# Kernel optimization log

Measured on AMD Instinct MI355X. Metric: run time of the kernel, lower is better.

## Reference

```python
import jax, jax.numpy as jnp
import numpy as np

IMAGE_SIZE = 256  # init kwarg image_size
BS, NCAM, N = 2, 3, 128


def _normalise_scale_factor(v):
    v = v / v.mean()
    sf = 0.2 / jnp.abs(v - 1.0).max()
    return jnp.where(sf < 1.0, (v - 1.0) * sf + 1.0, v)


def setup_inputs() -> dict:
    key = jax.random.key(0)
    ks = jax.random.split(key, 7)
    S = IMAGE_SIZE
    # 2D projected points in pixel coords [0, S)
    points = jax.random.uniform(ks[0], (BS, NCAM, N, 2), dtype=jnp.float32) * S
    # per-point render params in the model's clamp ranges
    sigmas = jax.random.uniform(ks[1], (BS, N), dtype=jnp.float32) * 0.06 + 0.041
    exponents = jax.random.uniform(ks[2], (BS, N), dtype=jnp.float32) * 1.5 + 0.5
    intensities = jax.random.uniform(ks[3], (BS, N), dtype=jnp.float32) * 0.6 + 0.41
    # per-camera scale factors near 1
    camera_sigmas = jax.random.uniform(ks[4], (BS, NCAM), dtype=jnp.float32) * 0.2 + 0.9
    camera_exponents = jax.random.uniform(ks[5], (BS, NCAM), dtype=jnp.float32) * 0.2 + 0.9
    camera_intensities = jax.random.uniform(ks[6], (BS, NCAM), dtype=jnp.float32) * 0.2 + 0.9
    return {
        'points': points, 'sigmas': sigmas, 'exponents': exponents,
        'intensities': intensities, 'camera_sigmas': camera_sigmas,
        'camera_exponents': camera_exponents, 'camera_intensities': camera_intensities,
    }


def reference(points, sigmas, exponents, intensities,
              camera_sigmas, camera_exponents, camera_intensities):
    S = IMAGE_SIZE
    bs, N = points.shape[0], points.shape[2]
    s2 = S // 2
    # normalise pixel coords to [-1, 1], flatten cameras into batch
    p = jnp.clip((points - s2) / s2, -1.0, 1.0).reshape(bs * 3, N, 2)
    # camera scale factors (normalised as in forward())
    cs = _normalise_scale_factor(camera_sigmas).reshape(bs * 3)
    ce = _normalise_scale_factor(camera_exponents).reshape(bs * 3)
    ci = _normalise_scale_factor(camera_intensities).reshape(bs * 3)
    # repeat_interleave(3, 0) over batch -> (bs*3, N, 1, 1)
    sig = (jnp.repeat(sigmas, 3, axis=0) * cs[:, None])[:, :, None, None]
    expn = (jnp.repeat(exponents, 3, axis=0) * ce[:, None])[:, :, None, None]
    inten = (jnp.repeat(intensities, 3, axis=0) * ci[:, None])[:, :, None, None]
    grid = jnp.linspace(-1.0, 1.0, S, dtype=jnp.float32)
    px = p[:, :, 0][:, :, None, None]  # (bs3, N, 1, 1)
    py = p[:, :, 1][:, :, None, None]
    # squared distance of every point to every pixel: (bs3, N, S, S)
    # y varies over axis -2 (rows), x over axis -1 (cols), matching meshgrid(ij)
    dst = (grid[None, None, None, :] - px) ** 2 + (grid[None, None, :, None] - py) ** 2
    blobs = jnp.exp(-(dst / (2.0 * sig ** 2)) ** expn)
    masks = jnp.minimum((blobs * inten).max(axis=1), 1.0)  # amax over N points
    masks = masks.reshape(bs, 3, S, S)
    blobs = blobs.reshape(bs, 3, N, S, S)
    return masks, blobs
```

## Files before the change

### kernel.cpp

```cpp
#include <hip/hip_runtime.h>

#define SZ   256
#define NPTS 128
#define NB3  6

__device__ __forceinline__ float norm6(const float* __restrict__ v, int idx) {
    float a0 = v[0], a1 = v[1], a2 = v[2], a3 = v[3], a4 = v[4], a5 = v[5];
    float mean = (a0 + a1 + a2 + a3 + a4 + a5) * (1.0f / 6.0f);
    float inv = 1.0f / mean;
    float b0 = a0 * inv, b1 = a1 * inv, b2 = a2 * inv;
    float b3 = a3 * inv, b4 = a4 * inv, b5 = a5 * inv;
    float d = fmaxf(fmaxf(fmaxf(fabsf(b0 - 1.f), fabsf(b1 - 1.f)),
                          fmaxf(fabsf(b2 - 1.f), fabsf(b3 - 1.f))),
                    fmaxf(fabsf(b4 - 1.f), fabsf(b5 - 1.f)));
    float sf = 0.2f / d;
    float vi = v[idx] * inv;
    return (sf < 1.0f) ? (vi - 1.0f) * sf + 1.0f : vi;
}

__global__ __launch_bounds__(256) void render_kernel(
    const float* __restrict__ points,
    const float* __restrict__ sigmas,
    const float* __restrict__ exponents,
    const float* __restrict__ intensities,
    const float* __restrict__ cam_s,
    const float* __restrict__ cam_e,
    const float* __restrict__ cam_i,
    float* __restrict__ masks,
    float* __restrict__ blobs)
{
    __shared__ float s_px[NPTS], s_py[NPTS], s_q[NPTS], s_e[NPTS], s_i[NPTS];

    const int b3  = blockIdx.x >> 6;
    const int yb  = (blockIdx.x & 63) << 2;
    const int tid = threadIdx.x;

    if (tid < NPTS) {
        const int b = b3 / 3;
        const float cs = norm6(cam_s, b3);
        const float ce = norm6(cam_e, b3);
        const float ci = norm6(cam_i, b3);
        float px = points[(b3 * NPTS + tid) * 2 + 0];
        float py = points[(b3 * NPTS + tid) * 2 + 1];
        px = fminf(fmaxf((px - 128.0f) * (1.0f / 128.0f), -1.0f), 1.0f);
        py = fminf(fmaxf((py - 128.0f) * (1.0f / 128.0f), -1.0f), 1.0f);
        const float sg = sigmas[b * NPTS + tid] * cs;
        s_px[tid] = px;
        s_py[tid] = py;
        s_q[tid]  = 1.0f / (2.0f * sg * sg);
        s_e[tid]  = exponents[b * NPTS + tid] * ce;
        s_i[tid]  = intensities[b * NPTS + tid] * ci;
    }
    __syncthreads();

    const int y  = yb + (tid >> 6);
    const int x0 = (tid & 63) << 2;
    const float gy  = -1.0f + (float)y * (2.0f / 255.0f);
    const float gx0 = -1.0f + (float)(x0    ) * (2.0f / 255.0f);
    const float gx1 = -1.0f + (float)(x0 + 1) * (2.0f / 255.0f);
    const float gx2 = -1.0f + (float)(x0 + 2) * (2.0f / 255.0f);
    const float gx3 = -1.0f + (float)(x0 + 3) * (2.0f / 255.0f);

    float m0 = 0.f, m1 = 0.f, m2 = 0.f, m3 = 0.f;
    float4* bptr = (float4*)(blobs + (size_t)b3 * NPTS * SZ * SZ
                                   + (size_t)y * SZ + x0);
    const size_t pstride = (SZ * SZ) / 4;

    #pragma unroll 4
    for (int n = 0; n < NPTS; ++n) {
        const float px = s_px[n], py = s_py[n];
        const float q  = s_q[n],  e  = s_e[n], it = s_i[n];
        const float dy  = gy - py;
        const float dy2 = dy * dy;
        const float d0 = gx0 - px, d1 = gx1 - px, d2 = gx2 - px, d3 = gx3 - px;
        const float u0 = fmaf(d0, d0, dy2) * q;
        const float u1 = fmaf(d1, d1, dy2) * q;
        const float u2 = fmaf(d2, d2, dy2) * q;
        const float u3 = fmaf(d3, d3, dy2) * q;
        const float bl0 = __expf(-__expf(e * __logf(u0)));
        const float bl1 = __expf(-__expf(e * __logf(u1)));
        const float bl2 = __expf(-__expf(e * __logf(u2)));
        const float bl3 = __expf(-__expf(e * __logf(u3)));
        bptr[(size_t)n * pstride] = make_float4(bl0, bl1, bl2, bl3);
        m0 = fmaxf(m0, bl0 * it);
        m1 = fmaxf(m1, bl1 * it);
        m2 = fmaxf(m2, bl2 * it);
        m3 = fmaxf(m3, bl3 * it);
    }

    float4* mptr = (float4*)(masks + (size_t)b3 * SZ * SZ + (size_t)y * SZ + x0);
    *mptr = make_float4(fminf(m0, 1.f), fminf(m1, 1.f),
                        fminf(m2, 1.f), fminf(m3, 1.f));
}

extern "C" void kernel_launch(void* const* d_in, const int* in_sizes, int n_in,
                              void* d_out, int out_size, void* d_ws, size_t ws_size,
                              hipStream_t stream) {
    const float* points      = (const float*)d_in[0];
    const float* sigmas      = (const float*)d_in[1];
    const float* exponents   = (const float*)d_in[2];
    const float* intensities = (const float*)d_in[3];
    const float* cam_s       = (const float*)d_in[4];
    const float* cam_e       = (const float*)d_in[5];
    const float* cam_i       = (const float*)d_in[6];

    float* out   = (float*)d_out;
    float* masks = out;
    float* blobs = out + NB3 * SZ * SZ;

    hipLaunchKernelGGL(render_kernel, dim3(NB3 * 64), dim3(256), 0, stream,
                       points, sigmas, exponents, intensities,
                       cam_s, cam_e, cam_i, masks, blobs);
}
```

Before: 217.9 us.

## Fold per-point constants into log2 domain and remap one pixel per thread

Rewrites the blob math in base 2 with hardware exp2/log2 builtins. The per-point scale q and the exponent are folded into a single additive constant so each pixel needs one fma, one log2 and two exp2. Point parameters are packed into a float4 in shared memory. Work is also remapped so each block handles one row and each thread one pixel with scalar stores, which raises block count fourfold but gives up float4 stores and per-thread amortisation. The kernel is bound by the blob writes (about 200 MB), so the gain in compute may matter less than the effect on store efficiency.

```diff
diff --git a/kernel.cpp b/kernel.cpp
--- a/kernel.cpp
+++ b/kernel.cpp
@@ -3,6 +3,9 @@
 #define SZ   256
 #define NPTS 128
 #define NB3  6
+
+#define EXP2F(x) __builtin_amdgcn_exp2f(x)
+#define LOG2F(x) __builtin_amdgcn_logf(x)
 
 __device__ __forceinline__ float norm6(const float* __restrict__ v, int idx) {
     float a0 = v[0], a1 = v[1], a2 = v[2], a3 = v[3], a4 = v[4], a5 = v[5];
@@ -29,10 +32,11 @@
     float* __restrict__ masks,
     float* __restrict__ blobs)
 {
-    __shared__ float s_px[NPTS], s_py[NPTS], s_q[NPTS], s_e[NPTS], s_i[NPTS];
+    __shared__ float4 s_p[NPTS];
+    __shared__ float  s_i[NPTS];
 
-    const int b3  = blockIdx.x >> 6;
-    const int yb  = (blockIdx.x & 63) << 2;
+    const int b3  = blockIdx.x >> 8;
+    const int y   = blockIdx.x & 255;
     const int tid = threadIdx.x;
 
     if (tid < NPTS) {
@@ -45,52 +49,35 @@
         px = fminf(fmaxf((px - 128.0f) * (1.0f / 128.0f), -1.0f), 1.0f);
         py = fminf(fmaxf((py - 128.0f) * (1.0f / 128.0f), -1.0f), 1.0f);
         const float sg = sigmas[b * NPTS + tid] * cs;
-        s_px[tid] = px;
-        s_py[tid] = py;
-        s_q[tid]  = 1.0f / (2.0f * sg * sg);
-        s_e[tid]  = exponents[b * NPTS + tid] * ce;
-        s_i[tid]  = intensities[b * NPTS + tid] * ci;
+        const float e  = exponents[b * NPTS + tid] * ce;
+        const float q  = 1.0f / (2.0f * sg * sg);
+        const float C  = 0.5287663729448977f;
+        const float c2 = fmaf(e, LOG2F(q), C);
+        s_p[tid] = make_float4(px, py, e, c2);
+        s_i[tid] = intensities[b * NPTS + tid] * ci;
     }
     __syncthreads();
 
-    const int y  = yb + (tid >> 6);
-    const int x0 = (tid & 63) << 2;
-    const float gy  = -1.0f + (float)y * (2.0f / 255.0f);
-    const float gx0 = -1.0f + (float)(x0    ) * (2.0f / 255.0f);
-    const float gx1 = -1.0f + (float)(x0 + 1) * (2.0f / 255.0f);
-    const float gx2 = -1.0f + (float)(x0 + 2) * (2.0f / 255.0f);
-    const float gx3 = -1.0f + (float)(x0 + 3) * (2.0f / 255.0f);
+    const float gy = -1.0f + (float)y   * (2.0f / 255.0f);
+    const float gx = -1.0f + (float)tid * (2.0f / 255.0f);
 
-    float m0 = 0.f, m1 = 0.f, m2 = 0.f, m3 = 0.f;
-    float4* bptr = (float4*)(blobs + (size_t)b3 * NPTS * SZ * SZ
-                                   + (size_t)y * SZ + x0);
-    const size_t pstride = (SZ * SZ) / 4;
+    float m = 0.0f;
+    float* bptr = blobs + (size_t)b3 * NPTS * SZ * SZ + (size_t)y * SZ + tid;
 
     #pragma unroll 4
     for (int n = 0; n < NPTS; ++n) {
-        const float px = s_px[n], py = s_py[n];
-        const float q  = s_q[n],  e  = s_e[n], it = s_i[n];
-        const float dy  = gy - py;
-        const float dy2 = dy * dy;
-        const float d0 = gx0 - px, d1 = gx1 - px, d2 = gx2 - px, d3 = gx3 - px;
-        const float u0 = fmaf(d0, d0, dy2) * q;
-        const float u1 = fmaf(d1, d1, dy2) * q;
-        const float u2 = fmaf(d2, d2, dy2) * q;
-        const float u3 = fmaf(d3, d3, dy2) * q;
-        const float bl0 = __expf(-__expf(e * __logf(u0)));
-        const float bl1 = __expf(-__expf(e * __logf(u1)));
-        const float bl2 = __expf(-__expf(e * __logf(u2)));
-        const float bl3 = __expf(-__expf(e * __logf(u3)));
-        bptr[(size_t)n * pstride] = make_float4(bl0, bl1, bl2, bl3);
-        m0 = fmaxf(m0, bl0 * it);
-        m1 = fmaxf(m1, bl1 * it);
-        m2 = fmaxf(m2, bl2 * it);
-        m3 = fmaxf(m3, bl3 * it);
+        const float4 p = s_p[n];
+        const float dx = gx - p.x;
+        const float dy = gy - p.y;
+        const float u  = fmaf(dx, dx, dy * dy);
+        const float l  = fmaf(p.z, LOG2F(u), p.w);
+        const float t  = EXP2F(l);
+        const float bl = EXP2F(-t);
+        bptr[(size_t)n * (SZ * SZ)] = bl;
+        m = fmaxf(m, bl * s_i[n]);
     }
 
-    float4* mptr = (float4*)(masks + (size_t)b3 * SZ * SZ + (size_t)y * SZ + x0);
-    *mptr = make_float4(fminf(m0, 1.f), fminf(m1, 1.f),
-                        fminf(m2, 1.f), fminf(m3, 1.f));
+    masks[(size_t)b3 * SZ * SZ + (size_t)y * SZ + tid] = fminf(m, 1.0f);
 }
 
 extern "C" void kernel_launch(void* const* d_in, const int* in_sizes, int n_in,
@@ -108,7 +95,7 @@
     float* masks = out;
     float* blobs = out + NB3 * SZ * SZ;
 
-    hipLaunchKernelGGL(render_kernel, dim3(NB3 * 64), dim3(256), 0, stream,
+    hipLaunchKernelGGL(render_kernel, dim3(NB3 * SZ), dim3(256), 0, stream,
                        points, sigmas, exponents, intensities,
                        cam_s, cam_e, cam_i, masks, blobs);
 }
```

New measurement: 207.4 us. -4.8%, faster.
